# Optimization experiments

Measured on AMD Instinct MI355X. Metric: run time of the kernel, lower is better.

## Reference

```python
import jax, jax.numpy as jnp
import numpy as np

C = 64; H = 80; W = 160; B = 3; L = 4
REC = [4, 3, 2]  # agents per scene, sum = 9
EPS = 1e-5
NEG = -1e30  # stands in for -inf (numerically identical after softmax)


def setup_inputs() -> dict:
    key = jax.random.key(0)
    ks = jax.random.split(key, 24)
    def p(i, shape, s=0.05):
        return s * jax.random.normal(ks[i], shape, jnp.float32)
    x = jax.random.normal(ks[0], (sum(REC), C, H, W), jnp.float32)
    mask = jnp.ones((B, L, H, W), jnp.float32)
    record_len = jnp.array(REC, jnp.int32)
    eye = jnp.broadcast_to(jnp.array([[1., 0., 0.], [0., 1., 0.]], jnp.float32), (B, L, L, 2, 3))
    noise = 0.05 * jax.random.normal(ks[1], (B, L, L, 2, 3), jnp.float32)
    diag = jnp.eye(L, dtype=bool)[None, :, :, None, None]
    pairwise_t_matrix = jnp.where(diag, eye, eye + noise)  # near-identity normalized affines
    inp = dict(x=x, mask=mask, record_len=record_len, pairwise_t_matrix=pairwise_t_matrix)
    chans = [(2 * C, 128), (128, 32), (32, 8)]
    for n, (ci, co) in zip([1, 2, 3], chans):
        inp[f'w{n}'] = p(2 * n, (ci, co))
        inp[f'cb{n}'] = p(2 * n + 1, (co,), 0.01)
        inp[f'g{n}'] = 1.0 + p(8 + n, (co,), 0.1)
        inp[f'be{n}'] = p(12 + n, (co,), 0.1)
        inp[f'rm{n}'] = jnp.zeros((co,), jnp.float32)
        inp[f'rv{n}'] = jnp.ones((co,), jnp.float32)
    inp['w4'] = p(16, (8, 1)); inp['cb4'] = p(17, (1,), 0.01)
    inp['mlp_w'] = p(18, (C, C)); inp['mlp_b'] = p(19, (C,), 0.01)
    return inp


def _bilinear(feat, px, py):
    # feat [C,H,W]; px,py [H,W] source pixel coords; zero padding outside
    x0 = jnp.floor(px); y0 = jnp.floor(py)
    wx = px - x0; wy = py - y0
    x0i = x0.astype(jnp.int32); y0i = y0.astype(jnp.int32)
    def gat(xi, yi):
        inb = ((xi >= 0) & (xi < W) & (yi >= 0) & (yi < H)).astype(feat.dtype)
        v = feat[:, jnp.clip(yi, 0, H - 1), jnp.clip(xi, 0, W - 1)]
        return v * inb
    return (gat(x0i, y0i) * (1 - wx) * (1 - wy) + gat(x0i + 1, y0i) * wx * (1 - wy)
            + gat(x0i, y0i + 1) * (1 - wx) * wy + gat(x0i + 1, y0i + 1) * wx * wy)


def _warp_one(feat, theta):
    # torch affine_grid convention: src_norm = theta @ [x_n, y_n, 1]
    ys = jnp.linspace(-1.0, 1.0, H); xs = jnp.linspace(-1.0, 1.0, W)
    gx, gy = jnp.meshgrid(xs, ys)  # [H,W]
    sx = theta[0, 0] * gx + theta[0, 1] * gy + theta[0, 2]
    sy = theta[1, 0] * gx + theta[1, 1] * gy + theta[1, 2]
    px = (sx + 1.0) * (W - 1) / 2.0
    py = (sy + 1.0) * (H - 1) / 2.0
    return _bilinear(feat, px, py)

_warp_j = jax.vmap(_warp_one, in_axes=(0, 0))        # over neighbor j
_warp_ij = jax.vmap(_warp_j, in_axes=(None, 0))      # over ego i
_warp_bij = jax.vmap(_warp_ij, in_axes=(0, 0))       # over scene b


def _forward(x, mask, rec, ptm, w1, cb1, g1, be1, rm1, rv1, w2, cb2, g2, be2, rm2, rv2,
             w3, cb3, g3, be3, rm3, rv3, w4, cb4, mlp_w, mlp_b):
    # regroup: pad per-scene agent features to [B,L,C,H,W]
    feats, idx = [], 0
    for n in rec:
        feats.append(jnp.pad(x[idx:idx + n], ((0, L - n), (0, 0), (0, 0), (0, 0))))
        idx += n
    node = jnp.stack(feats)                                      # [B,L,C,H,W]
    valid = jnp.asarray((np.asarray(rec)[:, None] > np.arange(L)).astype(np.float32))  # [B,L]
    theta = jnp.swapaxes(ptm, 1, 2)                              # theta[b,i,j] = ptm[b,j,i]
    nbr = _warp_bij(node, theta)                                 # [B,L,L,C,H,W]
    wm = _warp_bij(mask[:, :, None], theta)                      # [B,L,L,1,H,W] warped ROI masks
    com_mask = wm * valid[:, None, :, None, None, None]
    ego = jnp.broadcast_to(node[:, :, None], nbr.shape)          # ego feature repeated over j
    z = jnp.concatenate([nbr, ego], axis=3)                      # [B,L,L,2C,H,W]

    def conv_bn_relu(t, w, cb, g, be, rm, rv):
        t = jnp.einsum('bijchw,co->bijohw', t, w) + cb[:, None, None]
        t = (t - rm[:, None, None]) * (g[:, None, None] / jnp.sqrt(rv[:, None, None] + EPS)) + be[:, None, None]
        return jax.nn.relu(t)

    h = conv_bn_relu(z, w1, cb1, g1, be1, rm1, rv1)
    h = conv_bn_relu(h, w2, cb2, g2, be2, rm2, rv2)
    h = conv_bn_relu(h, w3, cb3, g3, be3, rm3, rv3)
    s = jax.nn.relu(jnp.einsum('bijchw,co->bijohw', h, w4) + cb4[:, None, None])  # [B,L,L,1,H,W]
    s = jnp.where(com_mask == 0, NEG, s)
    aw = jax.nn.softmax(s, axis=2)                               # softmax over neighbors j
    updated = jnp.sum(aw * nbr * com_mask, axis=2)               # [B,L,C,H,W]
    out = updated[:, 0]                                          # ego agent per scene [B,C,H,W]
    return jnp.einsum('bchw,cd->bdhw', out, mlp_w) + mlp_b[:, None, None]


def reference(x, mask, record_len, pairwise_t_matrix, w1, cb1, g1, be1, rm1, rv1,
              w2, cb2, g2, be2, rm2, rv2, w3, cb3, g3, be3, rm3, rv3, w4, cb4, mlp_w, mlp_b):
    rec = [int(v) for v in np.asarray(record_len)]
    return _forward(x, mask, rec, pairwise_t_matrix, w1, cb1, g1, be1, rm1, rv1,
                    w2, cb2, g2, be2, rm2, rv2, w3, cb3, g3, be3, rm3, rv3, w4, cb4, mlp_w, mlp_b)
```

## Files before the change

### kernel.cpp

```cpp
#include <hip/hip_runtime.h>
#include <math.h>

#define CC 64
#define HH 80
#define WW 160
#define BB 3
#define LL 4
#define HW (HH * WW)
#define EPSf 1e-5f
#define NEGf -1e30f

typedef __attribute__((ext_vector_type(8))) short bf16x8;
typedef __attribute__((ext_vector_type(4))) float f32x4;

union BU { unsigned short s[8]; bf16x8 v; };

__device__ __forceinline__ unsigned short f2bf(float f) {
    unsigned int u = __float_as_uint(f);
    u = u + 0x7fffu + ((u >> 16) & 1u);
    return (unsigned short)(u >> 16);
}
__device__ __forceinline__ float b2f(unsigned short h) {
    return __uint_as_float(((unsigned int)h) << 16);
}

__device__ __forceinline__ void src_xy(const float* __restrict__ th, int pix,
                                       float& px, float& py) {
    int w = pix % WW, h = pix / WW;
    float gx = -1.f + 2.f * (float)w / (float)(WW - 1);
    float gy = -1.f + 2.f * (float)h / (float)(HH - 1);
    float sx = th[0] * gx + th[1] * gy + th[2];
    float sy = th[3] * gx + th[4] * gy + th[5];
    px = (sx + 1.f) * (float)(WW - 1) * 0.5f;
    py = (sy + 1.f) * (float)(HH - 1) * 0.5f;
}

struct Tap { int a00, a01, a10, a11; float w00, w01, w10, w11; };

__device__ __forceinline__ Tap mk_tap(float px, float py) {
    Tap tp;
    float x0f = floorf(px), y0f = floorf(py);
    float wx = px - x0f, wy = py - y0f;
    int x0 = (int)x0f, y0 = (int)y0f, x1 = x0 + 1, y1 = y0 + 1;
    float bx0 = (x0 >= 0 && x0 < WW) ? 1.f : 0.f;
    float bx1 = (x1 >= 0 && x1 < WW) ? 1.f : 0.f;
    float by0 = (y0 >= 0 && y0 < HH) ? 1.f : 0.f;
    float by1 = (y1 >= 0 && y1 < HH) ? 1.f : 0.f;
    int xc0 = min(max(x0, 0), WW - 1), xc1 = min(max(x1, 0), WW - 1);
    int yc0 = min(max(y0, 0), HH - 1), yc1 = min(max(y1, 0), HH - 1);
    tp.w00 = (1.f - wx) * (1.f - wy) * bx0 * by0;
    tp.w01 = wx * (1.f - wy) * bx1 * by0;
    tp.w10 = (1.f - wx) * wy * bx0 * by1;
    tp.w11 = wx * wy * bx1 * by1;
    tp.a00 = yc0 * WW + xc0; tp.a01 = yc0 * WW + xc1;
    tp.a10 = yc1 * WW + xc0; tp.a11 = yc1 * WW + xc1;
    return tp;
}


__global__ __launch_bounds__(256) void k_prep(
    const float* __restrict__ w1, const float* __restrict__ w2,
    const float* __restrict__ mlpw,
    const float* __restrict__ cb1, const float* __restrict__ g1,
    const float* __restrict__ be1, const float* __restrict__ rm1, const float* __restrict__ rv1,
    const float* __restrict__ cb2, const float* __restrict__ g2,
    const float* __restrict__ be2, const float* __restrict__ rm2, const float* __restrict__ rv2,
    const float* __restrict__ cb3, const float* __restrict__ g3,
    const float* __restrict__ be3, const float* __restrict__ rm3, const float* __restrict__ rv3,
    unsigned short* __restrict__ w1T, unsigned short* __restrict__ w2T,
    unsigned short* __restrict__ mwT,
    float* __restrict__ kk1, float* __restrict__ bb1,
    float* __restrict__ kk2, float* __restrict__ bb2,
    float* __restrict__ kk3, float* __restrict__ bb3)
{
    int idx = blockIdx.x * 256 + threadIdx.x;
    if (idx < 16384) {
        int o = idx >> 7, c = idx & 127;
        w1T[idx] = f2bf(w1[c * 128 + o]);
    } else if (idx < 20480) {
        int i = idx - 16384;
        int o2 = i >> 7, o = i & 127;
        w2T[i] = f2bf(w2[o * 32 + o2]);
    } else if (idx < 24576) {
        int i = idx - 20480;
        int d = i >> 6, c = i & 63;
        mwT[i] = f2bf(mlpw[c * 64 + d]);
    } else if (idx < 24704) {
        int o = idx - 24576;
        float k = g1[o] * rsqrtf(rv1[o] + EPSf);
        kk1[o] = k; bb1[o] = fmaf(cb1[o] - rm1[o], k, be1[o]);
    } else if (idx < 24736) {
        int o = idx - 24704;
        float k = g2[o] * rsqrtf(rv2[o] + EPSf);
        kk2[o] = k; bb2[o] = fmaf(cb2[o] - rm2[o], k, be2[o]);
    } else if (idx < 24744) {
        int o = idx - 24736;
        float k = g3[o] * rsqrtf(rv3[o] + EPSf);
        kk3[o] = k; bb3[o] = fmaf(cb3[o] - rm3[o], k, be3[o]);
    }
}


__global__ __launch_bounds__(256, 5) void k_fused(
    const float* __restrict__ x, const float* __restrict__ mask,
    const int* __restrict__ rec, const float* __restrict__ ptm,
    const unsigned short* __restrict__ w1T, const unsigned short* __restrict__ w2T,
    const unsigned short* __restrict__ mwT,
    const float* __restrict__ kk1, const float* __restrict__ bb1,
    const float* __restrict__ kk2, const float* __restrict__ bb2,
    const float* __restrict__ kk3, const float* __restrict__ bb3,
    const float* __restrict__ w3, const float* __restrict__ w4,
    const float* __restrict__ cb4, const float* __restrict__ mlp_b,
    float* __restrict__ out)
{
    __shared__ __align__(16) char pool[27136];
    unsigned short* nbr_s = (unsigned short*)pool;
    unsigned short* H1s   = (unsigned short*)(pool + 9216);
    float* s_s   = (float*)(pool + 26624);
    float* com_s = (float*)(pool + 26880);

    int t = threadIdx.x;
    int b = blockIdx.x / 800, tile = blockIdx.x % 800;
    int pix0 = tile * 16;
    int wave = t >> 6, lane = t & 63, q = lane >> 4, r16 = lane & 15;
    int pix = pix0 + r16;

    int r0 = rec[0], r1 = rec[1], r2 = rec[2];
    int rb = (b == 0) ? r0 : ((b == 1) ? r1 : r2);
    int off = (b >= 1 ? r0 : 0) + (b >= 2 ? r1 : 0);
    bool valid = (wave < rb);

    unsigned short* Hw = H1s + wave * (16 * 136);
    float* H2w = (float*)Hw;
    const f32x4 z4 = {0.f, 0.f, 0.f, 0.f};

    if (valid) {
        const float* th = ptm + (size_t)(b * 4 + wave) * 24;
        float px_, py_; src_xy(th, pix, px_, py_);
        Tap tp = mk_tap(px_, py_);
        const float* feat = x + (size_t)(off + wave) * CC * HW;
        BU u0, u1;
        #pragma unroll
        for (int i = 0; i < 8; ++i) {
            const float* f0 = feat + (size_t)(q * 8 + i) * HW;
            float v0 = tp.w00 * f0[tp.a00] + tp.w01 * f0[tp.a01]
                     + tp.w10 * f0[tp.a10] + tp.w11 * f0[tp.a11];
            u0.s[i] = f2bf(v0);
            const float* f1 = feat + (size_t)(32 + q * 8 + i) * HW;
            float v1 = tp.w00 * f1[tp.a00] + tp.w01 * f1[tp.a01]
                     + tp.w10 * f1[tp.a10] + tp.w11 * f1[tp.a11];
            u1.s[i] = f2bf(v1);
        }
        float wm = 0.f;
        if (q == 0) {
            const float* mk = mask + (size_t)(b * 4 + wave) * HW;
            wm = tp.w00 * mk[tp.a00] + tp.w01 * mk[tp.a01]
               + tp.w10 * mk[tp.a10] + tp.w11 * mk[tp.a11];
        }
        *(bf16x8*)&nbr_s[(wave * 16 + r16) * 72 + q * 8]      = u0.v;
        *(bf16x8*)&nbr_s[(wave * 16 + r16) * 72 + 32 + q * 8] = u1.v;

        BU v0u, v1u;
        const float* xe = x + (size_t)off * CC * HW + pix;
        #pragma unroll
        for (int i = 0; i < 8; ++i) {
            v0u.s[i] = f2bf(xe[(size_t)(q * 8 + i) * HW]);
            v1u.s[i] = f2bf(xe[(size_t)(32 + q * 8 + i) * HW]);
        }

        f32x4 acc1[8];
        #pragma unroll
        for (int nt = 0; nt < 8; ++nt) acc1[nt] = z4;
        #pragma unroll
        for (int ks = 0; ks < 4; ++ks) {
            bf16x8 A = (ks == 0) ? u0.v : (ks == 1) ? u1.v : (ks == 2) ? v0u.v : v1u.v;
            int kcol = ks * 32 + q * 8;
            #pragma unroll
            for (int nt = 0; nt < 8; ++nt) {
                bf16x8 bw = *(const bf16x8*)(w1T + (size_t)(nt * 16 + r16) * 128 + kcol);
                acc1[nt] = __builtin_amdgcn_mfma_f32_16x16x32_bf16(A, bw, acc1[nt], 0, 0, 0);
            }
        }
        #pragma unroll
        for (int nt = 0; nt < 8; ++nt) {
            int o = nt * 16 + r16;
            float kv = kk1[o], bv = bb1[o];
            #pragma unroll
            for (int r = 0; r < 4; ++r) {
                float h = fmaxf(fmaf(acc1[nt][r], kv, bv), 0.f);
                Hw[(q * 4 + r) * 136 + o] = f2bf(h);
            }
        }

        f32x4 acc2[2]; acc2[0] = z4; acc2[1] = z4;
        #pragma unroll
        for (int ks = 0; ks < 4; ++ks) {
            int kcol = ks * 32 + q * 8;
            bf16x8 A = *(const bf16x8*)&Hw[r16 * 136 + kcol];
            #pragma unroll
            for (int nt = 0; nt < 2; ++nt) {
                bf16x8 bw = *(const bf16x8*)(w2T + (size_t)(nt * 16 + r16) * 128 + kcol);
                acc2[nt] = __builtin_amdgcn_mfma_f32_16x16x32_bf16(A, bw, acc2[nt], 0, 0, 0);
            }
        }
        #pragma unroll
        for (int nt = 0; nt < 2; ++nt) {
            int o = nt * 16 + r16;
            float kv = kk2[o], bv = bb2[o];
            #pragma unroll
            for (int r = 0; r < 4; ++r) {
                float h = fmaxf(fmaf(acc2[nt][r], kv, bv), 0.f);
                H2w[(q * 4 + r) * 36 + o] = h;
            }
        }

        if (q == 0) {
            float a3[8];
            #pragma unroll
            for (int o = 0; o < 8; ++o) a3[o] = 0.f;
            #pragma unroll 4
            for (int c = 0; c < 32; ++c) {
                float hv = H2w[r16 * 36 + c];
                #pragma unroll
                for (int o = 0; o < 8; ++o) a3[o] = fmaf(hv, w3[c * 8 + o], a3[o]);
            }
            float s = cb4[0];
            #pragma unroll
            for (int o = 0; o < 8; ++o) {
                float h = fmaxf(fmaf(a3[o], kk3[o], bb3[o]), 0.f);
                s = fmaf(h, w4[o], s);
            }
            s = fmaxf(s, 0.f);
            s_s[wave * 16 + r16]   = (wm == 0.f) ? NEGf : s;
            com_s[wave * 16 + r16] = wm;
        }
    } else {
        bf16x8 zb = {0, 0, 0, 0, 0, 0, 0, 0};
        *(bf16x8*)&nbr_s[(wave * 16 + r16) * 72 + q * 8]      = zb;
        *(bf16x8*)&nbr_s[(wave * 16 + r16) * 72 + 32 + q * 8] = zb;
        if (q == 0) { s_s[wave * 16 + r16] = NEGf; com_s[wave * 16 + r16] = 0.f; }
    }
    __syncthreads();

    float sj[4], cj[4];
    #pragma unroll
    for (int j = 0; j < 4; ++j) { sj[j] = s_s[j * 16 + r16]; cj[j] = com_s[j * 16 + r16]; }
    float m = fmaxf(fmaxf(sj[0], sj[1]), fmaxf(sj[2], sj[3]));
    float e[4], sum = 0.f;
    #pragma unroll
    for (int j = 0; j < 4; ++j) { e[j] = __expf(sj[j] - m); sum += e[j]; }
    float inv = 1.f / sum;
    float wgt[4];
    #pragma unroll
    for (int j = 0; j < 4; ++j) wgt[j] = e[j] * inv * cj[j];

    float uf0[8], uf1[8];
    #pragma unroll
    for (int i = 0; i < 8; ++i) { uf0[i] = 0.f; uf1[i] = 0.f; }
    #pragma unroll
    for (int j = 0; j < 4; ++j) {
        float wj = wgt[j];
        bf16x8 n0 = *(const bf16x8*)&nbr_s[(j * 16 + r16) * 72 + q * 8];
        bf16x8 n1 = *(const bf16x8*)&nbr_s[(j * 16 + r16) * 72 + 32 + q * 8];
        #pragma unroll
        for (int i = 0; i < 8; ++i) {
            uf0[i] = fmaf(wj, b2f((unsigned short)n0[i]), uf0[i]);
            uf1[i] = fmaf(wj, b2f((unsigned short)n1[i]), uf1[i]);
        }
    }
    BU p0, p1;
    #pragma unroll
    for (int i = 0; i < 8; ++i) { p0.s[i] = f2bf(uf0[i]); p1.s[i] = f2bf(uf1[i]); }

    f32x4 acc3 = z4;
    #pragma unroll
    for (int ks = 0; ks < 2; ++ks) {
        bf16x8 A = ks ? p1.v : p0.v;
        bf16x8 bw = *(const bf16x8*)(mwT + (size_t)(wave * 16 + r16) * 64 + ks * 32 + q * 8);
        acc3 = __builtin_amdgcn_mfma_f32_16x16x32_bf16(A, bw, acc3, 0, 0, 0);
    }
    __syncthreads();

    float* outT = (float*)pool;
    {
        int d = wave * 16 + r16;
        float mb = mlp_b[d];
        #pragma unroll
        for (int r = 0; r < 4; ++r)
            outT[d * 20 + q * 4 + r] = acc3[r] + mb;
    }
    __syncthreads();
    {
        int d = t >> 2, c4 = (t & 3) * 4;
        float4 v = *(const float4*)&outT[d * 20 + c4];
        *(float4*)&out[((size_t)(b * CC + d)) * HW + pix0 + c4] = v;
    }
}


extern "C" void kernel_launch(void* const* d_in, const int* in_sizes, int n_in,
                              void* d_out, int out_size, void* d_ws, size_t ws_size,
                              hipStream_t stream)
{
    const float* x    = (const float*)d_in[0];
    const float* mask = (const float*)d_in[1];
    const int*   rec  = (const int*)  d_in[2];
    const float* ptm  = (const float*)d_in[3];
    const float* w1   = (const float*)d_in[4];
    const float* cb1  = (const float*)d_in[5];
    const float* g1   = (const float*)d_in[6];
    const float* be1  = (const float*)d_in[7];
    const float* rm1  = (const float*)d_in[8];
    const float* rv1  = (const float*)d_in[9];
    const float* w2   = (const float*)d_in[10];
    const float* cb2  = (const float*)d_in[11];
    const float* g2   = (const float*)d_in[12];
    const float* be2  = (const float*)d_in[13];
    const float* rm2  = (const float*)d_in[14];
    const float* rv2  = (const float*)d_in[15];
    const float* w3   = (const float*)d_in[16];
    const float* cb3  = (const float*)d_in[17];
    const float* g3   = (const float*)d_in[18];
    const float* be3  = (const float*)d_in[19];
    const float* rm3  = (const float*)d_in[20];
    const float* rv3  = (const float*)d_in[21];
    const float* w4   = (const float*)d_in[22];
    const float* cb4  = (const float*)d_in[23];
    const float* mlpw = (const float*)d_in[24];
    const float* mlpb = (const float*)d_in[25];
    float* out = (float*)d_out;

    unsigned short* w1T = (unsigned short*)d_ws;
    unsigned short* w2T = w1T + 16384;
    unsigned short* mwT = w2T + 4096;
    float* kk1 = (float*)(mwT + 4096);
    float* bb1 = kk1 + 128;
    float* kk2 = bb1 + 128;
    float* bb2 = kk2 + 32;
    float* kk3 = bb2 + 32;
    float* bb3 = kk3 + 8;

    k_prep<<<dim3(97), dim3(256), 0, stream>>>(
        w1, w2, mlpw, cb1, g1, be1, rm1, rv1, cb2, g2, be2, rm2, rv2,
        cb3, g3, be3, rm3, rv3, w1T, w2T, mwT, kk1, bb1, kk2, bb2, kk3, bb3);

    k_fused<<<dim3(2400), dim3(256), 0, stream>>>(
        x, mask, rec, ptm, w1T, w2T, mwT,
        kk1, bb1, kk2, bb2, kk3, bb3,
        w3, w4, cb4, mlpb, out);
}
```

Baseline: 181.7 us.

## Process 32 pixels per block with two M-tiles and swizzled block order

Each block now handles 32 pixels instead of 16, with each wave running two 16-row MFMA tiles through conv1 so every w1T B-fragment load is reused twice. Warping and ego loading move into a cooperative prologue, with the ego features staged in a shared buffer, and the final MLP and output stores are split across waves by half-channels and pixel tiles. The block index is remapped across 8 groups to spread scenes and tiles, and the grid is halved. In exchange, LDS use nearly doubles and launch bounds drop to 3 blocks per CU, which lowers occupancy for a kernel that is dominated by gather loads.

```diff
diff --git a/kernel.cpp b/kernel.cpp
--- a/kernel.cpp
+++ b/kernel.cpp
@@ -101,7 +101,7 @@
 }
 
 
-__global__ __launch_bounds__(256, 5) void k_fused(
+__global__ __launch_bounds__(256, 3) void k_fused(
     const float* __restrict__ x, const float* __restrict__ mask,
     const int* __restrict__ rec, const float* __restrict__ ptm,
     const unsigned short* __restrict__ w1T, const unsigned short* __restrict__ w2T,
@@ -113,138 +113,162 @@
     const float* __restrict__ cb4, const float* __restrict__ mlp_b,
     float* __restrict__ out)
 {
-    __shared__ __align__(16) char pool[27136];
+    __shared__ __align__(16) char pool[50688];
     unsigned short* nbr_s = (unsigned short*)pool;
-    unsigned short* H1s   = (unsigned short*)(pool + 9216);
-    float* s_s   = (float*)(pool + 26624);
-    float* com_s = (float*)(pool + 26880);
+    unsigned short* ego_s = (unsigned short*)(pool + 18432);
+    unsigned short* H1s   = (unsigned short*)(pool + 23040);
+    float* H2s   = (float*)(pool + 40448);
+    float* s_s   = (float*)(pool + 49664);
+    float* com_s = (float*)(pool + 50176);
 
     int t = threadIdx.x;
-    int b = blockIdx.x / 800, tile = blockIdx.x % 800;
-    int pix0 = tile * 16;
+    int bid = blockIdx.x;
+    int work = (bid & 7) * 150 + (bid >> 3);
+    int b = work / 400, tile = work % 400;
+    int pix0 = tile * 32;
+
     int wave = t >> 6, lane = t & 63, q = lane >> 4, r16 = lane & 15;
-    int pix = pix0 + r16;
 
     int r0 = rec[0], r1 = rec[1], r2 = rec[2];
     int rb = (b == 0) ? r0 : ((b == 1) ? r1 : r2);
     int off = (b >= 1 ? r0 : 0) + (b >= 2 ? r1 : 0);
-    bool valid = (wave < rb);
-
-    unsigned short* Hw = H1s + wave * (16 * 136);
-    float* H2w = (float*)Hw;
+    bool validw = (wave < rb);
+
+    {
+        int pxA = lane & 31, cb = lane >> 5;
+        int pix = pix0 + pxA;
+        if (validw) {
+            const float* th = ptm + (size_t)(b * 4 + wave) * 24;
+            float fx, fy; src_xy(th, pix, fx, fy);
+            Tap tp = mk_tap(fx, fy);
+            if (cb == 0) {
+                const float* mk = mask + (size_t)(b * 4 + wave) * HW;
+                float wm = tp.w00 * mk[tp.a00] + tp.w01 * mk[tp.a01]
+                         + tp.w10 * mk[tp.a10] + tp.w11 * mk[tp.a11];
+                com_s[wave * 32 + pxA] = wm;
+            }
+            const float* feat = x + (size_t)(off + wave) * CC * HW;
+            unsigned short* dst = nbr_s + (size_t)(wave * 32 + pxA) * 72;
+            #pragma unroll
+            for (int i8 = 0; i8 < 4; ++i8) {
+                BU pk;
+                #pragma unroll
+                for (int i = 0; i < 8; ++i) {
+                    const float* f = feat + (size_t)(cb * 32 + i8 * 8 + i) * HW;
+                    pk.s[i] = f2bf(tp.w00 * f[tp.a00] + tp.w01 * f[tp.a01]
+                                 + tp.w10 * f[tp.a10] + tp.w11 * f[tp.a11]);
+                }
+                *(bf16x8*)(dst + cb * 32 + i8 * 8) = pk.v;
+            }
+        } else {
+            bf16x8 zb = {0,0,0,0,0,0,0,0};
+            unsigned short* dst = nbr_s + (size_t)(wave * 32 + pxA) * 72;
+            #pragma unroll
+            for (int i8 = 0; i8 < 4; ++i8)
+                *(bf16x8*)(dst + cb * 32 + i8 * 8) = zb;
+            if (cb == 0) { s_s[wave * 32 + pxA] = NEGf; com_s[wave * 32 + pxA] = 0.f; }
+        }
+        int pxe = t & 31, cb8 = t >> 5;
+        const float* xe = x + (size_t)off * CC * HW + pix0 + pxe;
+        BU pk;
+        #pragma unroll
+        for (int i = 0; i < 8; ++i)
+            pk.s[i] = f2bf(xe[(size_t)(cb8 * 8 + i) * HW]);
+        *(bf16x8*)(ego_s + (size_t)pxe * 72 + cb8 * 8) = pk.v;
+    }
+    __syncthreads();
+
     const f32x4 z4 = {0.f, 0.f, 0.f, 0.f};
-
-    if (valid) {
-        const float* th = ptm + (size_t)(b * 4 + wave) * 24;
-        float px_, py_; src_xy(th, pix, px_, py_);
-        Tap tp = mk_tap(px_, py_);
-        const float* feat = x + (size_t)(off + wave) * CC * HW;
-        BU u0, u1;
-        #pragma unroll
-        for (int i = 0; i < 8; ++i) {
-            const float* f0 = feat + (size_t)(q * 8 + i) * HW;
-            float v0 = tp.w00 * f0[tp.a00] + tp.w01 * f0[tp.a01]
-                     + tp.w10 * f0[tp.a10] + tp.w11 * f0[tp.a11];
-            u0.s[i] = f2bf(v0);
-            const float* f1 = feat + (size_t)(32 + q * 8 + i) * HW;
-            float v1 = tp.w00 * f1[tp.a00] + tp.w01 * f1[tp.a01]
-                     + tp.w10 * f1[tp.a10] + tp.w11 * f1[tp.a11];
-            u1.s[i] = f2bf(v1);
-        }
-        float wm = 0.f;
-        if (q == 0) {
-            const float* mk = mask + (size_t)(b * 4 + wave) * HW;
-            wm = tp.w00 * mk[tp.a00] + tp.w01 * mk[tp.a01]
-               + tp.w10 * mk[tp.a10] + tp.w11 * mk[tp.a11];
-        }
-        *(bf16x8*)&nbr_s[(wave * 16 + r16) * 72 + q * 8]      = u0.v;
-        *(bf16x8*)&nbr_s[(wave * 16 + r16) * 72 + 32 + q * 8] = u1.v;
-
-        BU v0u, v1u;
-        const float* xe = x + (size_t)off * CC * HW + pix;
-        #pragma unroll
-        for (int i = 0; i < 8; ++i) {
-            v0u.s[i] = f2bf(xe[(size_t)(q * 8 + i) * HW]);
-            v1u.s[i] = f2bf(xe[(size_t)(32 + q * 8 + i) * HW]);
-        }
-
-        f32x4 acc1[8];
-        #pragma unroll
-        for (int nt = 0; nt < 8; ++nt) acc1[nt] = z4;
+    if (validw) {
+        unsigned short* H1w = H1s + wave * (16 * 136);
+        float* H2w = H2s + wave * (16 * 36);
+
+        f32x4 acc[2][8];
+        #pragma unroll
+        for (int mt = 0; mt < 2; ++mt)
+            #pragma unroll
+            for (int nt = 0; nt < 8; ++nt) acc[mt][nt] = z4;
+
         #pragma unroll
         for (int ks = 0; ks < 4; ++ks) {
-            bf16x8 A = (ks == 0) ? u0.v : (ks == 1) ? u1.v : (ks == 2) ? v0u.v : v1u.v;
-            int kcol = ks * 32 + q * 8;
+            int kcol = (ks & 1) * 32 + q * 8;
+            const unsigned short* base = (ks < 2)
+                ? (nbr_s + (size_t)(wave * 32) * 72) : ego_s;
+            bf16x8 A0 = *(const bf16x8*)(base + (size_t)r16 * 72 + kcol);
+            bf16x8 A1 = *(const bf16x8*)(base + (size_t)(16 + r16) * 72 + kcol);
             #pragma unroll
             for (int nt = 0; nt < 8; ++nt) {
-                bf16x8 bw = *(const bf16x8*)(w1T + (size_t)(nt * 16 + r16) * 128 + kcol);
-                acc1[nt] = __builtin_amdgcn_mfma_f32_16x16x32_bf16(A, bw, acc1[nt], 0, 0, 0);
-            }
-        }
-        #pragma unroll
-        for (int nt = 0; nt < 8; ++nt) {
-            int o = nt * 16 + r16;
-            float kv = kk1[o], bv = bb1[o];
-            #pragma unroll
-            for (int r = 0; r < 4; ++r) {
-                float h = fmaxf(fmaf(acc1[nt][r], kv, bv), 0.f);
-                Hw[(q * 4 + r) * 136 + o] = f2bf(h);
-            }
-        }
-
-        f32x4 acc2[2]; acc2[0] = z4; acc2[1] = z4;
-        #pragma unroll
-        for (int ks = 0; ks < 4; ++ks) {
-            int kcol = ks * 32 + q * 8;
-            bf16x8 A = *(const bf16x8*)&Hw[r16 * 136 + kcol];
+                bf16x8 bw = *(const bf16x8*)(w1T + (size_t)(nt * 16 + r16) * 128
+                                             + ks * 32 + q * 8);
+                acc[0][nt] = __builtin_amdgcn_mfma_f32_16x16x32_bf16(A0, bw, acc[0][nt], 0, 0, 0);
+                acc[1][nt] = __builtin_amdgcn_mfma_f32_16x16x32_bf16(A1, bw, acc[1][nt], 0, 0, 0);
+            }
+        }
+
+        #pragma unroll
+        for (int mt = 0; mt < 2; ++mt) {
+            #pragma unroll
+            for (int nt = 0; nt < 8; ++nt) {
+                int o = nt * 16 + r16;
+                float kv = kk1[o], bv = bb1[o];
+                #pragma unroll
+                for (int r = 0; r < 4; ++r) {
+                    float h = fmaxf(fmaf(acc[mt][nt][r], kv, bv), 0.f);
+                    H1w[(q * 4 + r) * 136 + o] = f2bf(h);
+                }
+            }
+            f32x4 acc2[2]; acc2[0] = z4; acc2[1] = z4;
+            #pragma unroll
+            for (int ks = 0; ks < 4; ++ks) {
+                int kcol = ks * 32 + q * 8;
+                bf16x8 A = *(const bf16x8*)&H1w[r16 * 136 + kcol];
+                #pragma unroll
+                for (int nt = 0; nt < 2; ++nt) {
+                    bf16x8 bw = *(const bf16x8*)(w2T + (size_t)(nt * 16 + r16) * 128 + kcol);
+                    acc2[nt] = __builtin_amdgcn_mfma_f32_16x16x32_bf16(A, bw, acc2[nt], 0, 0, 0);
+                }
+            }
             #pragma unroll
             for (int nt = 0; nt < 2; ++nt) {
-                bf16x8 bw = *(const bf16x8*)(w2T + (size_t)(nt * 16 + r16) * 128 + kcol);
-                acc2[nt] = __builtin_amdgcn_mfma_f32_16x16x32_bf16(A, bw, acc2[nt], 0, 0, 0);
-            }
-        }
-        #pragma unroll
-        for (int nt = 0; nt < 2; ++nt) {
-            int o = nt * 16 + r16;
-            float kv = kk2[o], bv = bb2[o];
-            #pragma unroll
-            for (int r = 0; r < 4; ++r) {
-                float h = fmaxf(fmaf(acc2[nt][r], kv, bv), 0.f);
-                H2w[(q * 4 + r) * 36 + o] = h;
-            }
-        }
-
-        if (q == 0) {
-            float a3[8];
-            #pragma unroll
-            for (int o = 0; o < 8; ++o) a3[o] = 0.f;
-            #pragma unroll 4
-            for (int c = 0; c < 32; ++c) {
-                float hv = H2w[r16 * 36 + c];
-                #pragma unroll
-                for (int o = 0; o < 8; ++o) a3[o] = fmaf(hv, w3[c * 8 + o], a3[o]);
-            }
-            float s = cb4[0];
-            #pragma unroll
-            for (int o = 0; o < 8; ++o) {
-                float h = fmaxf(fmaf(a3[o], kk3[o], bb3[o]), 0.f);
-                s = fmaf(h, w4[o], s);
-            }
-            s = fmaxf(s, 0.f);
-            s_s[wave * 16 + r16]   = (wm == 0.f) ? NEGf : s;
-            com_s[wave * 16 + r16] = wm;
-        }
-    } else {
-        bf16x8 zb = {0, 0, 0, 0, 0, 0, 0, 0};
-        *(bf16x8*)&nbr_s[(wave * 16 + r16) * 72 + q * 8]      = zb;
-        *(bf16x8*)&nbr_s[(wave * 16 + r16) * 72 + 32 + q * 8] = zb;
-        if (q == 0) { s_s[wave * 16 + r16] = NEGf; com_s[wave * 16 + r16] = 0.f; }
+                int o = nt * 16 + r16;
+                float kv = kk2[o], bv = bb2[o];
+                #pragma unroll
+                for (int r = 0; r < 4; ++r) {
+                    float h = fmaxf(fmaf(acc2[nt][r], kv, bv), 0.f);
+                    H2w[(q * 4 + r) * 36 + o] = h;
+                }
+            }
+            if (q == 0) {
+                float a3[8];
+                #pragma unroll
+                for (int o = 0; o < 8; ++o) a3[o] = 0.f;
+                #pragma unroll 4
+                for (int c = 0; c < 32; ++c) {
+                    float hv = H2w[r16 * 36 + c];
+                    #pragma unroll
+                    for (int o = 0; o < 8; ++o) a3[o] = fmaf(hv, w3[c * 8 + o], a3[o]);
+                }
+                float s = cb4[0];
+                #pragma unroll
+                for (int o = 0; o < 8; ++o) {
+                    float h = fmaxf(fmaf(a3[o], kk3[o], bb3[o]), 0.f);
+                    s = fmaf(h, w4[o], s);
+                }
+                s = fmaxf(s, 0.f);
+                int pxs = mt * 16 + r16;
+                float wm = com_s[wave * 32 + pxs];
+                s_s[wave * 32 + pxs] = (wm == 0.f) ? NEGf : s;
+            }
+        }
     }
     __syncthreads();
 
+    int mt = wave & 1, nh = wave >> 1;
+    int px = mt * 16 + r16;
+
     float sj[4], cj[4];
     #pragma unroll
-    for (int j = 0; j < 4; ++j) { sj[j] = s_s[j * 16 + r16]; cj[j] = com_s[j * 16 + r16]; }
+    for (int j = 0; j < 4; ++j) { sj[j] = s_s[j * 32 + px]; cj[j] = com_s[j * 32 + px]; }
     float m = fmaxf(fmaxf(sj[0], sj[1]), fmaxf(sj[2], sj[3]));
     float e[4], sum = 0.f;
     #pragma unroll
@@ -260,8 +284,8 @@
     #pragma unroll
     for (int j = 0; j < 4; ++j) {
         float wj = wgt[j];
-        bf16x8 n0 = *(const bf16x8*)&nbr_s[(j * 16 + r16) * 72 + q * 8];
-        bf16x8 n1 = *(const bf16x8*)&nbr_s[(j * 16 + r16) * 72 + 32 + q * 8];
+        bf16x8 n0 = *(const bf16x8*)&nbr_s[(size_t)(j * 32 + px) * 72 + q * 8];
+        bf16x8 n1 = *(const bf16x8*)&nbr_s[(size_t)(j * 32 + px) * 72 + 32 + q * 8];
         #pragma unroll
         for (int i = 0; i < 8; ++i) {
             uf0[i] = fmaf(wj, b2f((unsigned short)n0[i]), uf0[i]);
@@ -272,28 +296,36 @@
     #pragma unroll
     for (int i = 0; i < 8; ++i) { p0.s[i] = f2bf(uf0[i]); p1.s[i] = f2bf(uf1[i]); }
 
-    f32x4 acc3 = z4;
+    f32x4 acc3[2]; acc3[0] = z4; acc3[1] = z4;
     #pragma unroll
     for (int ks = 0; ks < 2; ++ks) {
         bf16x8 A = ks ? p1.v : p0.v;
-        bf16x8 bw = *(const bf16x8*)(mwT + (size_t)(wave * 16 + r16) * 64 + ks * 32 + q * 8);
-        acc3 = __builtin_amdgcn_mfma_f32_16x16x32_bf16(A, bw, acc3, 0, 0, 0);
+        #pragma unroll
+        for (int nt = 0; nt < 2; ++nt) {
+            bf16x8 bw = *(const bf16x8*)(mwT + (size_t)(nh * 32 + nt * 16 + r16) * 64
+                                         + ks * 32 + q * 8);
+            acc3[nt] = __builtin_amdgcn_mfma_f32_16x16x32_bf16(A, bw, acc3[nt], 0, 0, 0);
+        }
     }
     __syncthreads();
 
     float* outT = (float*)pool;
-    {
-        int d = wave * 16 + r16;
+    #pragma unroll
+    for (int nt = 0; nt < 2; ++nt) {
+        int d = nh * 32 + nt * 16 + r16;
         float mb = mlp_b[d];
         #pragma unroll
         for (int r = 0; r < 4; ++r)
-            outT[d * 20 + q * 4 + r] = acc3[r] + mb;
+            outT[d * 36 + mt * 16 + q * 4 + r] = acc3[nt][r] + mb;
     }
     __syncthreads();
     {
-        int d = t >> 2, c4 = (t & 3) * 4;
-        float4 v = *(const float4*)&outT[d * 20 + c4];
-        *(float4*)&out[((size_t)(b * CC + d)) * HW + pix0 + c4] = v;
+        int d = t >> 2, c8 = (t & 3) * 8;
+        float4 v0 = *(const float4*)&outT[d * 36 + c8];
+        float4 v1 = *(const float4*)&outT[d * 36 + c8 + 4];
+        float* op = out + ((size_t)(b * CC + d)) * HW + pix0 + c8;
+        *(float4*)op = v0;
+        *(float4*)(op + 4) = v1;
     }
 }
 
@@ -344,7 +376,7 @@
         w1, w2, mlpw, cb1, g1, be1, rm1, rv1, cb2, g2, be2, rm2, rv2,
         cb3, g3, be3, rm3, rv3, w1T, w2T, mwT, kk1, bb1, kk2, bb2, kk3, bb3);
 
-    k_fused<<<dim3(2400), dim3(256), 0, stream>>>(
+    k_fused<<<dim3(1200), dim3(256), 0, stream>>>(
         x, mask, rec, ptm, w1T, w2T, mwT,
         kk1, bb1, kk2, bb2, kk3, bb3,
         w3, w4, cb4, mlpb, out);
```

Result: faster. 167.1 us (-8.0%).

## Stage ego features once in shared memory, batch gather loads, swizzle block order

Applied to the files above, without the earlier changes.

Previously each valid wave loaded and converted the ego agent's 64 channels for its 16-pixel tile on its own. Now the whole block loads them once into shared memory, reusing the hidden-layer buffer region, and the first GEMM reads its A operands from shared memory. The bilinear gather is reorganised to issue all four taps for eight channels before combining them, which exposes more memory-level parallelism. Block indices are remapped with a stride-8 swizzle, and the occupancy hint rises from 5 to 6 blocks per SM. The cost is an extra barrier and first-layer MFMAs now running for invalid waves, which are kept uniform so the barrier can be shared.

```diff
diff --git a/kernel.cpp b/kernel.cpp
--- a/kernel.cpp
+++ b/kernel.cpp
@@ -101,7 +101,7 @@
 }
 
 
-__global__ __launch_bounds__(256, 5) void k_fused(
+__global__ __launch_bounds__(256, 6) void k_fused(
     const float* __restrict__ x, const float* __restrict__ mask,
     const int* __restrict__ rec, const float* __restrict__ ptm,
     const unsigned short* __restrict__ w1T, const unsigned short* __restrict__ w2T,
@@ -115,72 +115,99 @@
 {
     __shared__ __align__(16) char pool[27136];
     unsigned short* nbr_s = (unsigned short*)pool;
-    unsigned short* H1s   = (unsigned short*)(pool + 9216);
+    unsigned short* Hbase = (unsigned short*)(pool + 9216);
+    unsigned short* ego_s = Hbase;
     float* s_s   = (float*)(pool + 26624);
     float* com_s = (float*)(pool + 26880);
 
     int t = threadIdx.x;
-    int b = blockIdx.x / 800, tile = blockIdx.x % 800;
+    int bid = blockIdx.x;
+    int work = (bid & 7) * 300 + (bid >> 3);
+    int b = work / 800, tile = work % 800;
     int pix0 = tile * 16;
+
     int wave = t >> 6, lane = t & 63, q = lane >> 4, r16 = lane & 15;
-    int pix = pix0 + r16;
 
     int r0 = rec[0], r1 = rec[1], r2 = rec[2];
     int rb = (b == 0) ? r0 : ((b == 1) ? r1 : r2);
     int off = (b >= 1 ? r0 : 0) + (b >= 2 ? r1 : 0);
-    bool valid = (wave < rb);
-
-    unsigned short* Hw = H1s + wave * (16 * 136);
-    float* H2w = (float*)Hw;
+    bool validw = (wave < rb);
+
+    {
+        int pix = pix0 + r16;
+        if (validw) {
+            const float* th = ptm + (size_t)(b * 4 + wave) * 24;
+            float fx, fy; src_xy(th, pix, fx, fy);
+            Tap tp = mk_tap(fx, fy);
+            if (q == 0) {
+                const float* mk = mask + (size_t)(b * 4 + wave) * HW;
+                float wm = tp.w00 * mk[tp.a00] + tp.w01 * mk[tp.a01]
+                         + tp.w10 * mk[tp.a10] + tp.w11 * mk[tp.a11];
+                com_s[wave * 16 + r16] = wm;
+            }
+            const float* feat = x + (size_t)(off + wave) * CC * HW;
+            const float* p00 = feat + tp.a00;
+            const float* p01 = feat + tp.a01;
+            const float* p10 = feat + tp.a10;
+            const float* p11 = feat + tp.a11;
+            unsigned short* dst = nbr_s + (size_t)(wave * 16 + r16) * 72 + q * 16;
+            #pragma unroll
+            for (int i8 = 0; i8 < 2; ++i8) {
+                float v00[8], v01[8], v10[8], v11[8];
+                #pragma unroll
+                for (int i = 0; i < 8; ++i) {
+                    size_t co = (size_t)(q * 16 + i8 * 8 + i) * HW;
+                    v00[i] = p00[co]; v01[i] = p01[co];
+                    v10[i] = p10[co]; v11[i] = p11[co];
+                }
+                BU pk;
+                #pragma unroll
+                for (int i = 0; i < 8; ++i)
+                    pk.s[i] = f2bf(tp.w00 * v00[i] + tp.w01 * v01[i]
+                                 + tp.w10 * v10[i] + tp.w11 * v11[i]);
+                *(bf16x8*)(dst + i8 * 8) = pk.v;
+            }
+        } else {
+            bf16x8 zb = {0,0,0,0,0,0,0,0};
+            unsigned short* dst = nbr_s + (size_t)(wave * 16 + r16) * 72 + q * 16;
+            *(bf16x8*)(dst)     = zb;
+            *(bf16x8*)(dst + 8) = zb;
+            if (q == 0) { s_s[wave * 16 + r16] = NEGf; com_s[wave * 16 + r16] = 0.f; }
+        }
+        int pxe = t & 15, cg = t >> 4;
+        const float* xe = x + (size_t)off * CC * HW + pix0 + pxe;
+        unsigned short tmp[4];
+        #pragma unroll
+        for (int i = 0; i < 4; ++i)
+            tmp[i] = f2bf(xe[(size_t)(cg * 4 + i) * HW]);
+        *(uint2*)(ego_s + (size_t)pxe * 72 + cg * 4) = *(const uint2*)tmp;
+    }
+    __syncthreads();
+
     const f32x4 z4 = {0.f, 0.f, 0.f, 0.f};
-
-    if (valid) {
-        const float* th = ptm + (size_t)(b * 4 + wave) * 24;
-        float px_, py_; src_xy(th, pix, px_, py_);
-        Tap tp = mk_tap(px_, py_);
-        const float* feat = x + (size_t)(off + wave) * CC * HW;
-        BU u0, u1;
-        #pragma unroll
-        for (int i = 0; i < 8; ++i) {
-            const float* f0 = feat + (size_t)(q * 8 + i) * HW;
-            float v0 = tp.w00 * f0[tp.a00] + tp.w01 * f0[tp.a01]
-                     + tp.w10 * f0[tp.a10] + tp.w11 * f0[tp.a11];
-            u0.s[i] = f2bf(v0);
-            const float* f1 = feat + (size_t)(32 + q * 8 + i) * HW;
-            float v1 = tp.w00 * f1[tp.a00] + tp.w01 * f1[tp.a01]
-                     + tp.w10 * f1[tp.a10] + tp.w11 * f1[tp.a11];
-            u1.s[i] = f2bf(v1);
-        }
-        float wm = 0.f;
-        if (q == 0) {
-            const float* mk = mask + (size_t)(b * 4 + wave) * HW;
-            wm = tp.w00 * mk[tp.a00] + tp.w01 * mk[tp.a01]
-               + tp.w10 * mk[tp.a10] + tp.w11 * mk[tp.a11];
-        }
-        *(bf16x8*)&nbr_s[(wave * 16 + r16) * 72 + q * 8]      = u0.v;
-        *(bf16x8*)&nbr_s[(wave * 16 + r16) * 72 + 32 + q * 8] = u1.v;
-
-        BU v0u, v1u;
-        const float* xe = x + (size_t)off * CC * HW + pix;
-        #pragma unroll
-        for (int i = 0; i < 8; ++i) {
-            v0u.s[i] = f2bf(xe[(size_t)(q * 8 + i) * HW]);
-            v1u.s[i] = f2bf(xe[(size_t)(32 + q * 8 + i) * HW]);
-        }
-
-        f32x4 acc1[8];
-        #pragma unroll
-        for (int nt = 0; nt < 8; ++nt) acc1[nt] = z4;
+    f32x4 acc1[8];
+    #pragma unroll
+    for (int nt = 0; nt < 8; ++nt) acc1[nt] = z4;
+    {
+        const unsigned short* nb = nbr_s + (size_t)(wave * 16) * 72;
         #pragma unroll
         for (int ks = 0; ks < 4; ++ks) {
-            bf16x8 A = (ks == 0) ? u0.v : (ks == 1) ? u1.v : (ks == 2) ? v0u.v : v1u.v;
-            int kcol = ks * 32 + q * 8;
+            int kcol = (ks & 1) * 32 + q * 8;
+            const unsigned short* base = (ks < 2) ? nb : ego_s;
+            bf16x8 A = *(const bf16x8*)(base + (size_t)r16 * 72 + kcol);
             #pragma unroll
             for (int nt = 0; nt < 8; ++nt) {
-                bf16x8 bw = *(const bf16x8*)(w1T + (size_t)(nt * 16 + r16) * 128 + kcol);
+                bf16x8 bw = *(const bf16x8*)(w1T + (size_t)(nt * 16 + r16) * 128
+                                             + ks * 32 + q * 8);
                 acc1[nt] = __builtin_amdgcn_mfma_f32_16x16x32_bf16(A, bw, acc1[nt], 0, 0, 0);
             }
         }
+    }
+    __syncthreads();
+
+    if (validw) {
+        unsigned short* H1w = Hbase + wave * (16 * 136);
+        float* H2w = (float*)H1w;
         #pragma unroll
         for (int nt = 0; nt < 8; ++nt) {
             int o = nt * 16 + r16;
@@ -188,15 +215,14 @@
             #pragma unroll
             for (int r = 0; r < 4; ++r) {
                 float h = fmaxf(fmaf(acc1[nt][r], kv, bv), 0.f);
-                Hw[(q * 4 + r) * 136 + o] = f2bf(h);
-            }
-        }
-
+                H1w[(q * 4 + r) * 136 + o] = f2bf(h);
+            }
+        }
         f32x4 acc2[2]; acc2[0] = z4; acc2[1] = z4;
         #pragma unroll
         for (int ks = 0; ks < 4; ++ks) {
             int kcol = ks * 32 + q * 8;
-            bf16x8 A = *(const bf16x8*)&Hw[r16 * 136 + kcol];
+            bf16x8 A = *(const bf16x8*)&H1w[r16 * 136 + kcol];
             #pragma unroll
             for (int nt = 0; nt < 2; ++nt) {
                 bf16x8 bw = *(const bf16x8*)(w2T + (size_t)(nt * 16 + r16) * 128 + kcol);
@@ -213,7 +239,6 @@
                 H2w[(q * 4 + r) * 36 + o] = h;
             }
         }
-
         if (q == 0) {
             float a3[8];
             #pragma unroll
@@ -231,14 +256,9 @@
                 s = fmaf(h, w4[o], s);
             }
             s = fmaxf(s, 0.f);
-            s_s[wave * 16 + r16]   = (wm == 0.f) ? NEGf : s;
-            com_s[wave * 16 + r16] = wm;
-        }
-    } else {
-        bf16x8 zb = {0, 0, 0, 0, 0, 0, 0, 0};
-        *(bf16x8*)&nbr_s[(wave * 16 + r16) * 72 + q * 8]      = zb;
-        *(bf16x8*)&nbr_s[(wave * 16 + r16) * 72 + 32 + q * 8] = zb;
-        if (q == 0) { s_s[wave * 16 + r16] = NEGf; com_s[wave * 16 + r16] = 0.f; }
+            float wm = com_s[wave * 16 + r16];
+            s_s[wave * 16 + r16] = (wm == 0.f) ? NEGf : s;
+        }
     }
     __syncthreads();
 
@@ -260,8 +280,8 @@
     #pragma unroll
     for (int j = 0; j < 4; ++j) {
         float wj = wgt[j];
-        bf16x8 n0 = *(const bf16x8*)&nbr_s[(j * 16 + r16) * 72 + q * 8];
-        bf16x8 n1 = *(const bf16x8*)&nbr_s[(j * 16 + r16) * 72 + 32 + q * 8];
+        bf16x8 n0 = *(const bf16x8*)&nbr_s[(size_t)(j * 16 + r16) * 72 + q * 8];
+        bf16x8 n1 = *(const bf16x8*)&nbr_s[(size_t)(j * 16 + r16) * 72 + 32 + q * 8];
         #pragma unroll
         for (int i = 0; i < 8; ++i) {
             uf0[i] = fmaf(wj, b2f((unsigned short)n0[i]), uf0[i]);
@@ -276,7 +296,8 @@
     #pragma unroll
     for (int ks = 0; ks < 2; ++ks) {
         bf16x8 A = ks ? p1.v : p0.v;
-        bf16x8 bw = *(const bf16x8*)(mwT + (size_t)(wave * 16 + r16) * 64 + ks * 32 + q * 8);
+        bf16x8 bw = *(const bf16x8*)(mwT + (size_t)(wave * 16 + r16) * 64
+                                     + ks * 32 + q * 8);
         acc3 = __builtin_amdgcn_mfma_f32_16x16x32_bf16(A, bw, acc3, 0, 0, 0);
     }
     __syncthreads();
```

After: 181.2 us. No clear change (-0.2%).
